# Kernel tuning notes

Measured on AMD Instinct MI355X. Metric: run time of the kernel, lower is better.

## Reference

```python
import jax, jax.numpy as jnp
import numpy as np

N_NODES = 100000
N_EDGES = 1600000
IN_F = 128
HID = 128
OUT_F = 40


def _gcn_conv(x, W, b, src, dst):
    # PyG GCNConv: h = x @ W; out[dst] += norm * h[src]; out += b
    n = x.shape[0]
    h = x @ W  # [N, out_channels]
    deg = jnp.zeros((n,), h.dtype).at[dst].add(jnp.ones((dst.shape[0],), h.dtype))
    dinv = jnp.where(deg > 0, jax.lax.rsqrt(deg), 0.0)  # deg^{-1/2}
    norm = dinv[src] * dinv[dst]  # [E+N]
    msg = h[src] * norm[:, None]  # [E+N, out_channels] gather
    out = jnp.zeros_like(h).at[dst].add(msg)  # scatter-add at targets
    if b is not None:
        out = out + b
    return out


def setup_inputs() -> dict:
    key = jax.random.key(0)
    k_x, k_e, k1, k2, k3, kb1, kb2 = jax.random.split(key, 7)
    x = jax.random.normal(k_x, (N_NODES, IN_F), dtype=jnp.float32)
    edge_index = jax.random.randint(k_e, (2, N_EDGES), 0, N_NODES, dtype=jnp.int64)
    s_in = 1.0 / np.sqrt(IN_F)
    s_h = 1.0 / np.sqrt(HID)
    W_in = jax.random.normal(k1, (IN_F, HID), dtype=jnp.float32) * s_in
    b_in = jnp.zeros((HID,), dtype=jnp.float32)
    W_mid = jax.random.normal(k2, (HID, HID), dtype=jnp.float32) * s_h
    b_mid = jnp.zeros((HID,), dtype=jnp.float32)
    W_out = jax.random.normal(k3, (HID, OUT_F), dtype=jnp.float32) * s_h
    return {"x": x, "edge_index": edge_index, "W_in": W_in, "b_in": b_in,
            "W_mid": W_mid, "b_mid": b_mid, "W_out": W_out}


def reference(x, edge_index, W_in, b_in, W_mid, b_mid, W_out):
    n = x.shape[0]
    loops = jnp.arange(n, dtype=edge_index.dtype)
    src = jnp.concatenate([edge_index[0], loops])  # add self-loops
    dst = jnp.concatenate([edge_index[1], loops])
    h = jax.nn.relu(_gcn_conv(x, W_in, b_in, src, dst))
    h = jax.nn.relu(_gcn_conv(h, W_mid, b_mid, src, dst))
    h = _gcn_conv(h, W_out, None, src, dst)  # out_conv: bias=False
    return jax.nn.log_softmax(h, axis=1)
```

## Files before the change

kernel.cpp:

```cpp
#include <hip/hip_runtime.h>
#include <math.h>

#define N_NODES 100000
#define N_EDGES 1600000
#define NBUCK 391
#define BSTRIDE 4608

typedef __attribute__((ext_vector_type(8))) _Float16 h8v;
typedef __attribute__((ext_vector_type(4))) float f32x4;
typedef __attribute__((ext_vector_type(2))) int i32x2;

#define GEMM_GRID 625
#define NTILES 3125


__global__ void k_prep(const int* __restrict__ srcv, const int* __restrict__ dstv,
                       int* __restrict__ bcnt, unsigned int* __restrict__ ebuf,
                       const float* __restrict__ x, const float* __restrict__ W1,
                       const float* __restrict__ W2, const float* __restrict__ W3,
                       _Float16* __restrict__ Wt,
                       _Float16* __restrict__ bufA, _Float16* __restrict__ bufB,
                       _Float16* __restrict__ zbuf) {
    const int tid = threadIdx.x;
    const int bid = blockIdx.x;

    if (bid < 625) {
        const int lane = tid & 63;
        const int wi = tid >> 6;
        const int nb = wi * 32;
        const int nn = lane & 15;
        const int quad = lane >> 4;
        const int kq = quad * 8;

        h8v bh[4][2], bl[4][2];
#pragma unroll
        for (int c = 0; c < 4; c++)
#pragma unroll
            for (int t = 0; t < 2; t++) {
#pragma unroll
                for (int j = 0; j < 8; j++) {
                    float w = W1[(c * 32 + kq + j) * 128 + nb + t * 16 + nn];
                    _Float16 hi = (_Float16)w;
                    bh[c][t][j] = hi;
                    bl[c][t][j] = (_Float16)(w - (float)hi);
                }
            }

        for (int rt = bid; rt < NTILES; rt += GEMM_GRID) {
            const int r0 = rt * 32;
            f32x4 acc[2][2] = {};
#pragma unroll
            for (int c = 0; c < 4; c++) {
                h8v a[2];
#pragma unroll
                for (int m = 0; m < 2; m++) {
                    const float* p = x + (size_t)(r0 + m * 16 + nn) * 128 + c * 32 + kq;
                    float4 p0 = *(const float4*)p;
                    float4 p1 = *(const float4*)(p + 4);
                    h8v av = {(_Float16)p0.x, (_Float16)p0.y, (_Float16)p0.z, (_Float16)p0.w,
                              (_Float16)p1.x, (_Float16)p1.y, (_Float16)p1.z, (_Float16)p1.w};
                    a[m] = av;
                }
#pragma unroll
                for (int m = 0; m < 2; m++)
#pragma unroll
                    for (int t = 0; t < 2; t++) {
                        acc[m][t] = __builtin_amdgcn_mfma_f32_16x16x32_f16(a[m], bh[c][t], acc[m][t], 0, 0, 0);
                        acc[m][t] = __builtin_amdgcn_mfma_f32_16x16x32_f16(a[m], bl[c][t], acc[m][t], 0, 0, 0);
                    }
            }
#pragma unroll
            for (int m = 0; m < 2; m++)
#pragma unroll
                for (int reg = 0; reg < 4; reg++) {
                    int r = r0 + m * 16 + quad * 4 + reg;
#pragma unroll
                    for (int t = 0; t < 2; t++)
                        bufA[(size_t)r * 128 + nb + t * 16 + nn] = (_Float16)acc[m][t][reg];
                }
        }
        return;
    }

    if (bid >= 1016) {
        if (bid == 1104) {
            if (tid < 128) {
                bufA[(size_t)N_NODES * 128 + tid] = (_Float16)0.f;
                bufB[(size_t)N_NODES * 128 + tid] = (_Float16)0.f;
            }
            if (tid < 64)  zbuf[(size_t)N_NODES * 64 + tid] = (_Float16)0.f;
            return;
        }
        int idx = (bid - 1016) * 256 + tid;
        if (idx >= 176 * 128) return;
        int n = idx / 128, k = idx % 128;
        _Float16 *ph, *pl;
        float v;
        if (n < 128) {
            v = W2[k * 128 + n];
            ph = Wt + 2 * 128 * 128; pl = Wt + 3 * 128 * 128;
        } else {
            int nloc = n - 128;
            v = (nloc < 40) ? W3[k * 40 + nloc] : 0.f;
            ph = Wt + 4 * 128 * 128; pl = Wt + 4 * 128 * 128 + 48 * 128;
            n = nloc;
        }
        _Float16 hi = (_Float16)v;
        _Float16 lo = (_Float16)(v - (float)hi);
        ph[n * 128 + k] = hi;
        pl[n * 128 + k] = lo;
        return;
    }

    __shared__ int hist[NBUCK];
    __shared__ int cur[NBUCK];
    for (int t = tid; t < NBUCK; t += 256) hist[t] = 0;
    __syncthreads();
    const int base = (bid - 625) * 4096;
#pragma unroll
    for (int i = 0; i < 16; i++) {
        int e = base + i * 256 + tid;
        if (e < N_EDGES) atomicAdd(&hist[dstv[e] >> 8], 1);
    }
    __syncthreads();
    for (int t = tid; t < NBUCK; t += 256)
        if (hist[t]) cur[t] = t * BSTRIDE + atomicAdd(&bcnt[t], hist[t]);
    __syncthreads();
#pragma unroll
    for (int i = 0; i < 16; i++) {
        int e = base + i * 256 + tid;
        if (e < N_EDGES) {
            int d = dstv[e];
            int p = atomicAdd(&cur[d >> 8], 1);
            ebuf[p] = ((unsigned int)srcv[e] << 8) | (unsigned int)(d & 255);
        }
    }
}


__launch_bounds__(256)
__global__ void k_bucket(const unsigned int* __restrict__ ebuf, const int* __restrict__ bcnt,
                         i32x2* __restrict__ rowse, float* __restrict__ dinv,
                         int* __restrict__ colidx, _Float16* __restrict__ bufA) {
    __shared__ int cnt[256];
    __shared__ int s[256];
    __shared__ int cur[256];
    __shared__ float sdv[256];
    const int tid = threadIdx.x;
    const int b = blockIdx.x;
    const int e0 = b * BSTRIDE;
    const int e1 = e0 + bcnt[b];
    cnt[tid] = 0;
    __syncthreads();
    for (int e = e0 + tid; e < e1; e += 256) atomicAdd(&cnt[ebuf[e] & 255u], 1);
    __syncthreads();
    int v = cnt[tid];
    int x = v;
    s[tid] = x;
    __syncthreads();
    for (int d = 1; d < 256; d <<= 1) {
        int t = (tid >= d) ? s[tid - d] : 0;
        __syncthreads();
        x += t;
        s[tid] = x;
        __syncthreads();
    }
    int start = e0 + x - v;
    int node = b * 256 + tid;
    float dvv = rsqrtf((float)(v + 1));
    sdv[tid] = dvv;
    if (node < N_NODES) {
        i32x2 se;
        se.x = start;
        se.y = start + v;
        rowse[node] = se;
        dinv[node] = dvv;
    }
    cur[tid] = start;
    __syncthreads();
    for (int e = e0 + tid; e < e1; e += 256) {
        unsigned int sd = ebuf[e];
        int pos = atomicAdd(&cur[sd & 255u], 1);
        colidx[pos] = (int)(sd >> 8);
    }
    __syncthreads();
    const int b0row = b * 256;
    const int chunk = tid & 15;
#pragma unroll
    for (int i = 0; i < 16; i++) {
        int rl = i * 16 + (tid >> 4);
        int row = b0row + rl;
        if (row < N_NODES) {
            _Float16* p = bufA + (size_t)row * 128 + chunk * 8;
            h8v vv = *(const h8v*)p;
            float d = sdv[rl];
            h8v o;
#pragma unroll
            for (int j = 0; j < 8; j++) o[j] = (_Float16)(d * (float)vv[j]);
            *(h8v*)p = o;
        }
    }
}


__launch_bounds__(256)
__global__ void k_fused128(const _Float16* __restrict__ hp, const i32x2* __restrict__ rowse,
                           const int* __restrict__ colidx, const float* __restrict__ bias,
                           const float* __restrict__ dinv,
                           const _Float16* __restrict__ Wthi, const _Float16* __restrict__ Wtlo,
                           _Float16* __restrict__ out) {
    __shared__ __align__(16) _Float16 As[16 * 128];
    const int lane = threadIdx.x & 63;
    const int wi = threadIdx.x >> 6;
    const int nn = lane & 15;
    const int quad = lane >> 4;
    const int r0 = blockIdx.x * 16;

    {
        const int rl = wi * 4 + quad;
        const int r = r0 + rl;
        const i32x2 se = rowse[r];
        const int deg = se.y - se.x;
        int m = deg;
        m = max(m, __shfl_xor(m, 16));
        m = max(m, __shfl_xor(m, 32));
        const _Float16* hpc = hp + nn * 8;
        h8v acc = {};
        for (int it = 0; it < m; it += 4) {
            int i0 = se.x + it;
            int s0 = colidx[i0];
            int s1 = colidx[i0 + 1];
            int s2 = colidx[i0 + 2];
            int s3 = colidx[i0 + 3];
            s0 = (it < deg) ? s0 : N_NODES;
            s1 = (it + 1 < deg) ? s1 : N_NODES;
            s2 = (it + 2 < deg) ? s2 : N_NODES;
            s3 = (it + 3 < deg) ? s3 : N_NODES;
            h8v v0 = *(const h8v*)(hpc + (size_t)s0 * 128);
            h8v v1 = *(const h8v*)(hpc + (size_t)s1 * 128);
            h8v v2 = *(const h8v*)(hpc + (size_t)s2 * 128);
            h8v v3 = *(const h8v*)(hpc + (size_t)s3 * 128);
            acc += v0;
            acc += v1;
            acc += v2;
            acc += v3;
        }
        h8v sv = *(const h8v*)(hpc + (size_t)r * 128);
        float dv = rsqrtf((float)(deg + 1));
        const float* bp = bias + nn * 8;
        float4 b0 = *(const float4*)bp;
        float4 b1 = *(const float4*)(bp + 4);
        float bb[8] = {b0.x, b0.y, b0.z, b0.w, b1.x, b1.y, b1.z, b1.w};
        h8v o;
#pragma unroll
        for (int j = 0; j < 8; j++) {
            float sx = (float)acc[j] + (float)sv[j];
            o[j] = (_Float16)fmaxf(fmaf(dv, sx, bb[j]), 0.f);
        }
        *(h8v*)(As + rl * 128 + ((nn ^ rl) * 8)) = o;
    }
    __syncthreads();

    const int nb = wi * 32;
    const int kq = quad * 8;
    f32x4 acc2[2] = {};
#pragma unroll
    for (int c = 0; c < 4; c++) {
        int ch = (c * 4 + quad) ^ nn;
        h8v a = *(const h8v*)(As + nn * 128 + ch * 8);
#pragma unroll
        for (int t = 0; t < 2; t++) {
            int off = (nb + t * 16 + nn) * 128 + c * 32 + kq;
            h8v bhv = *(const h8v*)(Wthi + off);
            h8v blv = *(const h8v*)(Wtlo + off);
            acc2[t] = __builtin_amdgcn_mfma_f32_16x16x32_f16(a, bhv, acc2[t], 0, 0, 0);
            acc2[t] = __builtin_amdgcn_mfma_f32_16x16x32_f16(a, blv, acc2[t], 0, 0, 0);
        }
    }
#pragma unroll
    for (int reg = 0; reg < 4; reg++) {
        int r = r0 + quad * 4 + reg;
        float dr = dinv[r];
#pragma unroll
        for (int t = 0; t < 2; t++)
            out[(size_t)r * 128 + nb + t * 16 + nn] = (_Float16)(acc2[t][reg] * dr);
    }
}

__launch_bounds__(256)
__global__ void k_fused40(const _Float16* __restrict__ hp, const i32x2* __restrict__ rowse,
                          const int* __restrict__ colidx, const float* __restrict__ bias,
                          const float* __restrict__ dinv,
                          const _Float16* __restrict__ Wthi, const _Float16* __restrict__ Wtlo,
                          _Float16* __restrict__ out) {
    __shared__ __align__(16) _Float16 As[16 * 128];
    const int lane = threadIdx.x & 63;
    const int wi = threadIdx.x >> 6;
    const int nn = lane & 15;
    const int quad = lane >> 4;
    const int r0 = blockIdx.x * 16;

    {
        const int rl = wi * 4 + quad;
        const int r = r0 + rl;
        const i32x2 se = rowse[r];
        const int deg = se.y - se.x;
        int m = deg;
        m = max(m, __shfl_xor(m, 16));
        m = max(m, __shfl_xor(m, 32));
        const _Float16* hpc = hp + nn * 8;
        h8v acc = {};
        for (int it = 0; it < m; it += 4) {
            int i0 = se.x + it;
            int s0 = colidx[i0];
            int s1 = colidx[i0 + 1];
            int s2 = colidx[i0 + 2];
            int s3 = colidx[i0 + 3];
            s0 = (it < deg) ? s0 : N_NODES;
            s1 = (it + 1 < deg) ? s1 : N_NODES;
            s2 = (it + 2 < deg) ? s2 : N_NODES;
            s3 = (it + 3 < deg) ? s3 : N_NODES;
            h8v v0 = *(const h8v*)(hpc + (size_t)s0 * 128);
            h8v v1 = *(const h8v*)(hpc + (size_t)s1 * 128);
            h8v v2 = *(const h8v*)(hpc + (size_t)s2 * 128);
            h8v v3 = *(const h8v*)(hpc + (size_t)s3 * 128);
            acc += v0;
            acc += v1;
            acc += v2;
            acc += v3;
        }
        h8v sv = *(const h8v*)(hpc + (size_t)r * 128);
        float dv = rsqrtf((float)(deg + 1));
        const float* bp = bias + nn * 8;
        float4 b0 = *(const float4*)bp;
        float4 b1 = *(const float4*)(bp + 4);
        float bb[8] = {b0.x, b0.y, b0.z, b0.w, b1.x, b1.y, b1.z, b1.w};
        h8v o;
#pragma unroll
        for (int j = 0; j < 8; j++) {
            float sx = (float)acc[j] + (float)sv[j];
            o[j] = (_Float16)fmaxf(fmaf(dv, sx, bb[j]), 0.f);
        }
        *(h8v*)(As + rl * 128 + ((nn ^ rl) * 8)) = o;
    }
    __syncthreads();

    if (wi < 3) {
        const int kq = quad * 8;
        f32x4 acc2 = {};
#pragma unroll
        for (int c = 0; c < 4; c++) {
            int ch = (c * 4 + quad) ^ nn;
            h8v a = *(const h8v*)(As + nn * 128 + ch * 8);
            int off = (wi * 16 + nn) * 128 + c * 32 + kq;
            h8v bhv = *(const h8v*)(Wthi + off);
            h8v blv = *(const h8v*)(Wtlo + off);
            acc2 = __builtin_amdgcn_mfma_f32_16x16x32_f16(a, bhv, acc2, 0, 0, 0);
            acc2 = __builtin_amdgcn_mfma_f32_16x16x32_f16(a, blv, acc2, 0, 0, 0);
        }
#pragma unroll
        for (int reg = 0; reg < 4; reg++) {
            int r = r0 + quad * 4 + reg;
            float dr = dinv[r];
            out[(size_t)r * 64 + wi * 16 + nn] = (_Float16)(acc2[reg] * dr);
        }
    }
}


__launch_bounds__(256)
__global__ void k_agg_out(const _Float16* __restrict__ hp, const i32x2* __restrict__ rowse,
                          const int* __restrict__ colidx, float* __restrict__ out) {
    const int lane = threadIdx.x & 63;
    const int wid = (blockIdx.x * blockDim.x + threadIdx.x) >> 6;
    const int rs = lane >> 3;
    const int cp = lane & 7;
    const int r = wid * 8 + rs;

    const i32x2 se = rowse[r];
    const int deg = se.y - se.x;
    int m = deg;
    m = max(m, __shfl_xor(m, 8));
    m = max(m, __shfl_xor(m, 16));
    m = max(m, __shfl_xor(m, 32));

    const _Float16* hpc = hp + cp * 8;
    h8v acc = {};
    for (int it = 0; it < m; it += 4) {
        int i0 = se.x + it;
        int s0 = colidx[i0];
        int s1 = colidx[i0 + 1];
        int s2 = colidx[i0 + 2];
        int s3 = colidx[i0 + 3];
        s0 = (it < deg) ? s0 : N_NODES;
        s1 = (it + 1 < deg) ? s1 : N_NODES;
        s2 = (it + 2 < deg) ? s2 : N_NODES;
        s3 = (it + 3 < deg) ? s3 : N_NODES;
        h8v v0 = *(const h8v*)(hpc + (size_t)s0 * 64);
        h8v v1 = *(const h8v*)(hpc + (size_t)s1 * 64);
        h8v v2 = *(const h8v*)(hpc + (size_t)s2 * 64);
        h8v v3 = *(const h8v*)(hpc + (size_t)s3 * 64);
        acc += v0;
        acc += v1;
        acc += v2;
        acc += v3;
    }

    h8v sv = *(const h8v*)(hpc + (size_t)r * 64);
    float dv = rsqrtf((float)(deg + 1));
    float z[8];
#pragma unroll
    for (int j = 0; j < 8; j++) z[j] = dv * ((float)acc[j] + (float)sv[j]);

    const bool act = cp < 5;
    float pm = -INFINITY;
    if (act) {
#pragma unroll
        for (int j = 0; j < 8; j++) pm = fmaxf(pm, z[j]);
    }
    pm = fmaxf(pm, __shfl_xor(pm, 1));
    pm = fmaxf(pm, __shfl_xor(pm, 2));
    pm = fmaxf(pm, __shfl_xor(pm, 4));
    float pe = 0.f;
    if (act) {
#pragma unroll
        for (int j = 0; j < 8; j++) pe += __expf(z[j] - pm);
    }
    pe += __shfl_xor(pe, 1);
    pe += __shfl_xor(pe, 2);
    pe += __shfl_xor(pe, 4);
    float lse = __logf(pe);
    if (act) {
        float* po = out + (size_t)r * 40 + cp * 8;
        float4 o0 = make_float4(z[0] - pm - lse, z[1] - pm - lse, z[2] - pm - lse, z[3] - pm - lse);
        float4 o1 = make_float4(z[4] - pm - lse, z[5] - pm - lse, z[6] - pm - lse, z[7] - pm - lse);
        *(float4*)po = o0;
        *(float4*)(po + 4) = o1;
    }
}


extern "C" void kernel_launch(void* const* d_in, const int* in_sizes, int n_in,
                              void* d_out, int out_size, void* d_ws, size_t ws_size,
                              hipStream_t stream) {
    const float* x     = (const float*)d_in[0];
    const int*   ei    = (const int*)d_in[1];
    const float* W_in  = (const float*)d_in[2];
    const float* b_in  = (const float*)d_in[3];
    const float* W_mid = (const float*)d_in[4];
    const float* b_mid = (const float*)d_in[5];
    const float* W_out = (const float*)d_in[6];
    float* out = (float*)d_out;

    const int* srcv = ei;
    const int* dstv = ei + N_EDGES;

    char* w = (char*)d_ws;
    float* dinv   = (float*)(w);
    i32x2* rowse  = (i32x2*)(w + (1ull << 19));
    int* bcnt     = (int*)(w + 1507328);
    int* colidx   = (int*)(w + (2ull << 20));
    unsigned int* ebuf = (unsigned int*)(w + (10ull << 20));
    _Float16* Wt  = (_Float16*)(w + (18ull << 20));
    _Float16* bufA = (_Float16*)(w + (19ull << 20));
    _Float16* bufB = (_Float16*)(w + (45ull << 20));
    _Float16* zbuf = (_Float16*)(w + (71ull << 20));

    _Float16* W2h = Wt + 2 * 128 * 128;
    _Float16* W2l = Wt + 3 * 128 * 128;
    _Float16* W3h = Wt + 4 * 128 * 128;
    _Float16* W3l = Wt + 4 * 128 * 128 + 48 * 128;

    (void)hipMemsetAsync(bcnt, 0, NBUCK * sizeof(int), stream);
    k_prep<<<1105, 256, 0, stream>>>(srcv, dstv, bcnt, ebuf, x, W_in, W_mid, W_out,
                                     Wt, bufA, bufB, zbuf);
    k_bucket<<<NBUCK, 256, 0, stream>>>(ebuf, bcnt, rowse, dinv, colidx, bufA);

    k_fused128<<<N_NODES / 16, 256, 0, stream>>>(bufA, rowse, colidx, b_in, dinv, W2h, W2l, bufB);
    k_fused40<<<N_NODES / 16, 256, 0, stream>>>(bufB, rowse, colidx, b_mid, dinv, W3h, W3l, zbuf);
    k_agg_out<<<N_NODES / 32, 256, 0, stream>>>(zbuf, rowse, colidx, out);
}
```

Before: 353.8 us.

## Split prep kernel and fold dinv scaling into first-layer GEMM epilogue

```diff
diff --git a/kernel.cpp b/kernel.cpp
--- a/kernel.cpp
+++ b/kernel.cpp
@@ -14,109 +14,52 @@
 #define NTILES 3125
 
 
-__global__ void k_prep(const int* __restrict__ srcv, const int* __restrict__ dstv,
-                       int* __restrict__ bcnt, unsigned int* __restrict__ ebuf,
-                       const float* __restrict__ x, const float* __restrict__ W1,
-                       const float* __restrict__ W2, const float* __restrict__ W3,
-                       _Float16* __restrict__ Wt,
+__launch_bounds__(256)
+__global__ void k_misc(const float* __restrict__ W2, const float* __restrict__ W3,
+                       _Float16* __restrict__ Wt, int* __restrict__ bcnt,
                        _Float16* __restrict__ bufA, _Float16* __restrict__ bufB,
                        _Float16* __restrict__ zbuf) {
     const int tid = threadIdx.x;
     const int bid = blockIdx.x;
-
-    if (bid < 625) {
-        const int lane = tid & 63;
-        const int wi = tid >> 6;
-        const int nb = wi * 32;
-        const int nn = lane & 15;
-        const int quad = lane >> 4;
-        const int kq = quad * 8;
-
-        h8v bh[4][2], bl[4][2];
-#pragma unroll
-        for (int c = 0; c < 4; c++)
-#pragma unroll
-            for (int t = 0; t < 2; t++) {
-#pragma unroll
-                for (int j = 0; j < 8; j++) {
-                    float w = W1[(c * 32 + kq + j) * 128 + nb + t * 16 + nn];
-                    _Float16 hi = (_Float16)w;
-                    bh[c][t][j] = hi;
-                    bl[c][t][j] = (_Float16)(w - (float)hi);
-                }
-            }
-
-        for (int rt = bid; rt < NTILES; rt += GEMM_GRID) {
-            const int r0 = rt * 32;
-            f32x4 acc[2][2] = {};
-#pragma unroll
-            for (int c = 0; c < 4; c++) {
-                h8v a[2];
-#pragma unroll
-                for (int m = 0; m < 2; m++) {
-                    const float* p = x + (size_t)(r0 + m * 16 + nn) * 128 + c * 32 + kq;
-                    float4 p0 = *(const float4*)p;
-                    float4 p1 = *(const float4*)(p + 4);
-                    h8v av = {(_Float16)p0.x, (_Float16)p0.y, (_Float16)p0.z, (_Float16)p0.w,
-                              (_Float16)p1.x, (_Float16)p1.y, (_Float16)p1.z, (_Float16)p1.w};
-                    a[m] = av;
-                }
-#pragma unroll
-                for (int m = 0; m < 2; m++)
-#pragma unroll
-                    for (int t = 0; t < 2; t++) {
-                        acc[m][t] = __builtin_amdgcn_mfma_f32_16x16x32_f16(a[m], bh[c][t], acc[m][t], 0, 0, 0);
-                        acc[m][t] = __builtin_amdgcn_mfma_f32_16x16x32_f16(a[m], bl[c][t], acc[m][t], 0, 0, 0);
-                    }
-            }
-#pragma unroll
-            for (int m = 0; m < 2; m++)
-#pragma unroll
-                for (int reg = 0; reg < 4; reg++) {
-                    int r = r0 + m * 16 + quad * 4 + reg;
-#pragma unroll
-                    for (int t = 0; t < 2; t++)
-                        bufA[(size_t)r * 128 + nb + t * 16 + nn] = (_Float16)acc[m][t][reg];
-                }
-        }
+    if (bid == 88) {
+        if (tid < 128) {
+            bufA[(size_t)N_NODES * 128 + tid] = (_Float16)0.f;
+            bufB[(size_t)N_NODES * 128 + tid] = (_Float16)0.f;
+        }
+        if (tid < 64)  zbuf[(size_t)N_NODES * 64 + tid] = (_Float16)0.f;
+        for (int t = tid; t < NBUCK; t += 256) bcnt[t] = 0;
         return;
     }
-
-    if (bid >= 1016) {
-        if (bid == 1104) {
-            if (tid < 128) {
-                bufA[(size_t)N_NODES * 128 + tid] = (_Float16)0.f;
-                bufB[(size_t)N_NODES * 128 + tid] = (_Float16)0.f;
-            }
-            if (tid < 64)  zbuf[(size_t)N_NODES * 64 + tid] = (_Float16)0.f;
-            return;
-        }
-        int idx = (bid - 1016) * 256 + tid;
-        if (idx >= 176 * 128) return;
-        int n = idx / 128, k = idx % 128;
-        _Float16 *ph, *pl;
-        float v;
-        if (n < 128) {
-            v = W2[k * 128 + n];
-            ph = Wt + 2 * 128 * 128; pl = Wt + 3 * 128 * 128;
-        } else {
-            int nloc = n - 128;
-            v = (nloc < 40) ? W3[k * 40 + nloc] : 0.f;
-            ph = Wt + 4 * 128 * 128; pl = Wt + 4 * 128 * 128 + 48 * 128;
-            n = nloc;
-        }
-        _Float16 hi = (_Float16)v;
-        _Float16 lo = (_Float16)(v - (float)hi);
-        ph[n * 128 + k] = hi;
-        pl[n * 128 + k] = lo;
-        return;
-    }
-
+    int idx = bid * 256 + tid;
+    if (idx >= 176 * 128) return;
+    int n = idx / 128, k = idx % 128;
+    _Float16 *ph, *pl;
+    float v;
+    if (n < 128) {
+        v = W2[k * 128 + n];
+        ph = Wt + 2 * 128 * 128; pl = Wt + 3 * 128 * 128;
+    } else {
+        int nloc = n - 128;
+        v = (nloc < 40) ? W3[k * 40 + nloc] : 0.f;
+        ph = Wt + 4 * 128 * 128; pl = Wt + 4 * 128 * 128 + 48 * 128;
+        n = nloc;
+    }
+    _Float16 hi = (_Float16)v;
+    _Float16 lo = (_Float16)(v - (float)hi);
+    ph[n * 128 + k] = hi;
+    pl[n * 128 + k] = lo;
+}
+
+
+__launch_bounds__(256)
+__global__ void k_bpart(const int* __restrict__ srcv, const int* __restrict__ dstv,
+                        int* __restrict__ bcnt, unsigned int* __restrict__ ebuf) {
     __shared__ int hist[NBUCK];
     __shared__ int cur[NBUCK];
+    const int tid = threadIdx.x;
     for (int t = tid; t < NBUCK; t += 256) hist[t] = 0;
     __syncthreads();
-    const int base = (bid - 625) * 4096;
+    const int base = blockIdx.x * 4096;
 #pragma unroll
     for (int i = 0; i < 16; i++) {
         int e = base + i * 256 + tid;
@@ -141,11 +84,10 @@
 __launch_bounds__(256)
 __global__ void k_bucket(const unsigned int* __restrict__ ebuf, const int* __restrict__ bcnt,
                          i32x2* __restrict__ rowse, float* __restrict__ dinv,
-                         int* __restrict__ colidx, _Float16* __restrict__ bufA) {
+                         int* __restrict__ colidx) {
     __shared__ int cnt[256];
     __shared__ int s[256];
     __shared__ int cur[256];
-    __shared__ float sdv[256];
     const int tid = threadIdx.x;
     const int b = blockIdx.x;
     const int e0 = b * BSTRIDE;
@@ -167,14 +109,12 @@
     }
     int start = e0 + x - v;
     int node = b * 256 + tid;
-    float dvv = rsqrtf((float)(v + 1));
-    sdv[tid] = dvv;
     if (node < N_NODES) {
         i32x2 se;
         se.x = start;
         se.y = start + v;
         rowse[node] = se;
-        dinv[node] = dvv;
+        dinv[node] = rsqrtf((float)(v + 1));
     }
     cur[tid] = start;
     __syncthreads();
@@ -183,22 +123,66 @@
         int pos = atomicAdd(&cur[sd & 255u], 1);
         colidx[pos] = (int)(sd >> 8);
     }
-    __syncthreads();
-    const int b0row = b * 256;
-    const int chunk = tid & 15;
-#pragma unroll
-    for (int i = 0; i < 16; i++) {
-        int rl = i * 16 + (tid >> 4);
-        int row = b0row + rl;
-        if (row < N_NODES) {
-            _Float16* p = bufA + (size_t)row * 128 + chunk * 8;
-            h8v vv = *(const h8v*)p;
-            float d = sdv[rl];
-            h8v o;
-#pragma unroll
-            for (int j = 0; j < 8; j++) o[j] = (_Float16)(d * (float)vv[j]);
-            *(h8v*)p = o;
-        }
+}
+
+
+__launch_bounds__(256, 2)
+__global__ void k_gemm128_f32(const float* __restrict__ x, const float* __restrict__ W1,
+                              const float* __restrict__ dinv, _Float16* __restrict__ out) {
+    const int lane = threadIdx.x & 63;
+    const int wi = threadIdx.x >> 6;
+    const int nb = wi * 32;
+    const int nn = lane & 15;
+    const int quad = lane >> 4;
+    const int kq = quad * 8;
+
+    h8v bh[4][2], bl[4][2];
+#pragma unroll
+    for (int c = 0; c < 4; c++)
+#pragma unroll
+        for (int t = 0; t < 2; t++) {
+#pragma unroll
+            for (int j = 0; j < 8; j++) {
+                float w = W1[(c * 32 + kq + j) * 128 + nb + t * 16 + nn];
+                _Float16 hi = (_Float16)w;
+                bh[c][t][j] = hi;
+                bl[c][t][j] = (_Float16)(w - (float)hi);
+            }
+        }
+
+    for (int rt = blockIdx.x; rt < NTILES; rt += GEMM_GRID) {
+        const int r0 = rt * 32;
+        f32x4 acc[2][2] = {};
+#pragma unroll
+        for (int c = 0; c < 4; c++) {
+            h8v a[2];
+#pragma unroll
+            for (int m = 0; m < 2; m++) {
+                const float* p = x + (size_t)(r0 + m * 16 + nn) * 128 + c * 32 + kq;
+                float4 p0 = *(const float4*)p;
+                float4 p1 = *(const float4*)(p + 4);
+                h8v av = {(_Float16)p0.x, (_Float16)p0.y, (_Float16)p0.z, (_Float16)p0.w,
+                          (_Float16)p1.x, (_Float16)p1.y, (_Float16)p1.z, (_Float16)p1.w};
+                a[m] = av;
+            }
+#pragma unroll
+            for (int m = 0; m < 2; m++)
+#pragma unroll
+                for (int t = 0; t < 2; t++) {
+                    acc[m][t] = __builtin_amdgcn_mfma_f32_16x16x32_f16(a[m], bh[c][t], acc[m][t], 0, 0, 0);
+                    acc[m][t] = __builtin_amdgcn_mfma_f32_16x16x32_f16(a[m], bl[c][t], acc[m][t], 0, 0, 0);
+                }
+        }
+#pragma unroll
+        for (int m = 0; m < 2; m++)
+#pragma unroll
+            for (int reg = 0; reg < 4; reg++) {
+                int r = r0 + m * 16 + quad * 4 + reg;
+                float dv = dinv[r];
+#pragma unroll
+                for (int t = 0; t < 2; t++)
+                    out[(size_t)r * 128 + nb + t * 16 + nn] = (_Float16)(acc[m][t][reg] * dv);
+            }
     }
 }
 
@@ -471,11 +455,10 @@
     _Float16* W3h = Wt + 4 * 128 * 128;
     _Float16* W3l = Wt + 4 * 128 * 128 + 48 * 128;
 
-    (void)hipMemsetAsync(bcnt, 0, NBUCK * sizeof(int), stream);
-    k_prep<<<1105, 256, 0, stream>>>(srcv, dstv, bcnt, ebuf, x, W_in, W_mid, W_out,
-                                     Wt, bufA, bufB, zbuf);
-    k_bucket<<<NBUCK, 256, 0, stream>>>(ebuf, bcnt, rowse, dinv, colidx, bufA);
-
+    k_misc<<<89, 256, 0, stream>>>(W_mid, W_out, Wt, bcnt, bufA, bufB, zbuf);
+    k_bpart<<<NBUCK, 256, 0, stream>>>(srcv, dstv, bcnt, ebuf);
+    k_bucket<<<NBUCK, 256, 0, stream>>>(ebuf, bcnt, rowse, dinv, colidx);
+    k_gemm128_f32<<<GEMM_GRID, 256, 0, stream>>>(x, W_in, dinv, bufA);
     k_fused128<<<N_NODES / 16, 256, 0, stream>>>(bufA, rowse, colidx, b_in, dinv, W2h, W2l, bufB);
     k_fused40<<<N_NODES / 16, 256, 0, stream>>>(bufB, rowse, colidx, b_mid, dinv, W3h, W3l, zbuf);
     k_agg_out<<<N_NODES / 32, 256, 0, stream>>>(zbuf, rowse, colidx, out);
```

Result: no change. 357.8 us (+1.1%).

## Move first-layer GEMM into bucket kernel and fuse dinv scaling

Applied to the files above, without the earlier changes.

```diff
diff --git a/kernel.cpp b/kernel.cpp
--- a/kernel.cpp
+++ b/kernel.cpp
@@ -14,76 +14,18 @@
 #define NTILES 3125
 
 
-__global__ void k_prep(const int* __restrict__ srcv, const int* __restrict__ dstv,
-                       int* __restrict__ bcnt, unsigned int* __restrict__ ebuf,
-                       const float* __restrict__ x, const float* __restrict__ W1,
-                       const float* __restrict__ W2, const float* __restrict__ W3,
-                       _Float16* __restrict__ Wt,
-                       _Float16* __restrict__ bufA, _Float16* __restrict__ bufB,
-                       _Float16* __restrict__ zbuf) {
+__launch_bounds__(256)
+__global__ void k_bpart(const int* __restrict__ srcv, const int* __restrict__ dstv,
+                        int* __restrict__ bcnt, unsigned int* __restrict__ ebuf,
+                        const float* __restrict__ W2, const float* __restrict__ W3,
+                        _Float16* __restrict__ Wt,
+                        _Float16* __restrict__ bufA, _Float16* __restrict__ bufB,
+                        _Float16* __restrict__ zbuf) {
     const int tid = threadIdx.x;
     const int bid = blockIdx.x;
 
-    if (bid < 625) {
-        const int lane = tid & 63;
-        const int wi = tid >> 6;
-        const int nb = wi * 32;
-        const int nn = lane & 15;
-        const int quad = lane >> 4;
-        const int kq = quad * 8;
-
-        h8v bh[4][2], bl[4][2];
-#pragma unroll
-        for (int c = 0; c < 4; c++)
-#pragma unroll
-            for (int t = 0; t < 2; t++) {
-#pragma unroll
-                for (int j = 0; j < 8; j++) {
-                    float w = W1[(c * 32 + kq + j) * 128 + nb + t * 16 + nn];
-                    _Float16 hi = (_Float16)w;
-                    bh[c][t][j] = hi;
-                    bl[c][t][j] = (_Float16)(w - (float)hi);
-                }
-            }
-
-        for (int rt = bid; rt < NTILES; rt += GEMM_GRID) {
-            const int r0 = rt * 32;
-            f32x4 acc[2][2] = {};
-#pragma unroll
-            for (int c = 0; c < 4; c++) {
-                h8v a[2];
-#pragma unroll
-                for (int m = 0; m < 2; m++) {
-                    const float* p = x + (size_t)(r0 + m * 16 + nn) * 128 + c * 32 + kq;
-                    float4 p0 = *(const float4*)p;
-                    float4 p1 = *(const float4*)(p + 4);
-                    h8v av = {(_Float16)p0.x, (_Float16)p0.y, (_Float16)p0.z, (_Float16)p0.w,
-                              (_Float16)p1.x, (_Float16)p1.y, (_Float16)p1.z, (_Float16)p1.w};
-                    a[m] = av;
-                }
-#pragma unroll
-                for (int m = 0; m < 2; m++)
-#pragma unroll
-                    for (int t = 0; t < 2; t++) {
-                        acc[m][t] = __builtin_amdgcn_mfma_f32_16x16x32_f16(a[m], bh[c][t], acc[m][t], 0, 0, 0);
-                        acc[m][t] = __builtin_amdgcn_mfma_f32_16x16x32_f16(a[m], bl[c][t], acc[m][t], 0, 0, 0);
-                    }
-            }
-#pragma unroll
-            for (int m = 0; m < 2; m++)
-#pragma unroll
-                for (int reg = 0; reg < 4; reg++) {
-                    int r = r0 + m * 16 + quad * 4 + reg;
-#pragma unroll
-                    for (int t = 0; t < 2; t++)
-                        bufA[(size_t)r * 128 + nb + t * 16 + nn] = (_Float16)acc[m][t][reg];
-                }
-        }
-        return;
-    }
-
-    if (bid >= 1016) {
-        if (bid == 1104) {
+    if (bid >= 391) {
+        if (bid == 479) {
             if (tid < 128) {
                 bufA[(size_t)N_NODES * 128 + tid] = (_Float16)0.f;
                 bufB[(size_t)N_NODES * 128 + tid] = (_Float16)0.f;
@@ -91,7 +33,7 @@
             if (tid < 64)  zbuf[(size_t)N_NODES * 64 + tid] = (_Float16)0.f;
             return;
         }
-        int idx = (bid - 1016) * 256 + tid;
+        int idx = (bid - 391) * 256 + tid;
         if (idx >= 176 * 128) return;
         int n = idx / 128, k = idx % 128;
         _Float16 *ph, *pl;
@@ -116,7 +58,7 @@
     __shared__ int cur[NBUCK];
     for (int t = tid; t < NBUCK; t += 256) hist[t] = 0;
     __syncthreads();
-    const int base = (bid - 625) * 4096;
+    const int base = bid * 4096;
 #pragma unroll
     for (int i = 0; i < 16; i++) {
         int e = base + i * 256 + tid;
@@ -141,7 +83,9 @@
 __launch_bounds__(256)
 __global__ void k_bucket(const unsigned int* __restrict__ ebuf, const int* __restrict__ bcnt,
                          i32x2* __restrict__ rowse, float* __restrict__ dinv,
-                         int* __restrict__ colidx, _Float16* __restrict__ bufA) {
+                         int* __restrict__ colidx,
+                         const float* __restrict__ x, const float* __restrict__ W1,
+                         _Float16* __restrict__ bufA) {
     __shared__ int cnt[256];
     __shared__ int s[256];
     __shared__ int cur[256];
@@ -155,17 +99,17 @@
     for (int e = e0 + tid; e < e1; e += 256) atomicAdd(&cnt[ebuf[e] & 255u], 1);
     __syncthreads();
     int v = cnt[tid];
-    int x = v;
-    s[tid] = x;
+    int x0 = v;
+    s[tid] = x0;
     __syncthreads();
     for (int d = 1; d < 256; d <<= 1) {
         int t = (tid >= d) ? s[tid - d] : 0;
         __syncthreads();
-        x += t;
-        s[tid] = x;
+        x0 += t;
+        s[tid] = x0;
         __syncthreads();
     }
-    int start = e0 + x - v;
+    int start = e0 + x0 - v;
     int node = b * 256 + tid;
     float dvv = rsqrtf((float)(v + 1));
     sdv[tid] = dvv;
@@ -183,22 +127,67 @@
         int pos = atomicAdd(&cur[sd & 255u], 1);
         colidx[pos] = (int)(sd >> 8);
     }
-    __syncthreads();
-    const int b0row = b * 256;
-    const int chunk = tid & 15;
-#pragma unroll
-    for (int i = 0; i < 16; i++) {
-        int rl = i * 16 + (tid >> 4);
-        int row = b0row + rl;
-        if (row < N_NODES) {
-            _Float16* p = bufA + (size_t)row * 128 + chunk * 8;
-            h8v vv = *(const h8v*)p;
-            float d = sdv[rl];
-            h8v o;
-#pragma unroll
-            for (int j = 0; j < 8; j++) o[j] = (_Float16)(d * (float)vv[j]);
-            *(h8v*)p = o;
-        }
+
+    const int lane = tid & 63;
+    const int wi = tid >> 6;
+    const int nb = wi * 32;
+    const int nn = lane & 15;
+    const int quad = lane >> 4;
+    const int kq = quad * 8;
+
+    h8v bh[4][2], bl[4][2];
+#pragma unroll
+    for (int c = 0; c < 4; c++)
+#pragma unroll
+        for (int t = 0; t < 2; t++) {
+#pragma unroll
+            for (int j = 0; j < 8; j++) {
+                float w = W1[(c * 32 + kq + j) * 128 + nb + t * 16 + nn];
+                _Float16 hi = (_Float16)w;
+                bh[c][t][j] = hi;
+                bl[c][t][j] = (_Float16)(w - (float)hi);
+            }
+        }
+
+#pragma unroll
+    for (int tile = 0; tile < 8; tile++) {
+        const int r0 = b * 256 + tile * 32;
+        if (r0 >= N_NODES) break;
+        f32x4 acc[2][2] = {};
+#pragma unroll
+        for (int c = 0; c < 4; c++) {
+            h8v a[2];
+#pragma unroll
+            for (int m = 0; m < 2; m++) {
+                int rl = r0 + m * 16 + nn;
+                rl = (rl < N_NODES) ? rl : (N_NODES - 1);
+                const float* p = x + (size_t)rl * 128 + c * 32 + kq;
+                float4 p0 = *(const float4*)p;
+                float4 p1 = *(const float4*)(p + 4);
+                h8v av = {(_Float16)p0.x, (_Float16)p0.y, (_Float16)p0.z, (_Float16)p0.w,
+                          (_Float16)p1.x, (_Float16)p1.y, (_Float16)p1.z, (_Float16)p1.w};
+                a[m] = av;
+            }
+#pragma unroll
+            for (int m = 0; m < 2; m++)
+#pragma unroll
+                for (int t = 0; t < 2; t++) {
+                    acc[m][t] = __builtin_amdgcn_mfma_f32_16x16x32_f16(a[m], bh[c][t], acc[m][t], 0, 0, 0);
+                    acc[m][t] = __builtin_amdgcn_mfma_f32_16x16x32_f16(a[m], bl[c][t], acc[m][t], 0, 0, 0);
+                }
+        }
+#pragma unroll
+        for (int m = 0; m < 2; m++)
+#pragma unroll
+            for (int reg = 0; reg < 4; reg++) {
+                int r = r0 + m * 16 + quad * 4 + reg;
+                if (r < N_NODES) {
+                    float dv = sdv[r - b * 256];
+#pragma unroll
+                    for (int t = 0; t < 2; t++)
+                        bufA[(size_t)r * 128 + nb + t * 16 + nn] = (_Float16)(acc[m][t][reg] * dv);
+                }
+            }
     }
 }
 
@@ -472,10 +461,9 @@
     _Float16* W3l = Wt + 4 * 128 * 128 + 48 * 128;
 
     (void)hipMemsetAsync(bcnt, 0, NBUCK * sizeof(int), stream);
-    k_prep<<<1105, 256, 0, stream>>>(srcv, dstv, bcnt, ebuf, x, W_in, W_mid, W_out,
-                                     Wt, bufA, bufB, zbuf);
-    k_bucket<<<NBUCK, 256, 0, stream>>>(ebuf, bcnt, rowse, dinv, colidx, bufA);
-
+    k_bpart<<<480, 256, 0, stream>>>(srcv, dstv, bcnt, ebuf, W_mid, W_out, Wt,
+                                     bufA, bufB, zbuf);
+    k_bucket<<<NBUCK, 256, 0, stream>>>(ebuf, bcnt, rowse, dinv, colidx, x, W_in, bufA);
     k_fused128<<<N_NODES / 16, 256, 0, stream>>>(bufA, rowse, colidx, b_in, dinv, W2h, W2l, bufB);
     k_fused40<<<N_NODES / 16, 256, 0, stream>>>(bufB, rowse, colidx, b_mid, dinv, W3h, W3l, zbuf);
     k_agg_out<<<N_NODES / 32, 256, 0, stream>>>(zbuf, rowse, colidx, out);
```

Result: no change. 358.7 us (+1.4%).
